# Performance work log

Measured on AMD Instinct MI355X. Metric: run time of the kernel, lower is better.

Reference implementation:

```python
import jax, jax.numpy as jnp
import numpy as np
from jax import lax

B, N, K, NCP = 4, 2048, 20, 400
EPS = 1e-5


def _bn(x, gamma, beta, axes):
    # training-mode batch norm (biased variance), channel axis = 1
    m = jnp.mean(x, axis=axes, keepdims=True)
    v = jnp.var(x, axis=axes, keepdims=True)
    shape = [1] * x.ndim
    shape[1] = -1
    return (x - m) * lax.rsqrt(v + EPS) * gamma.reshape(shape) + beta.reshape(shape)


def _knn_idx(x, k):
    # x: [B, C, N] -> idx [B, N, k] (nearest, includes self like torch.cdist+topk(largest=False))
    x2 = jnp.sum(x * x, axis=1)  # [B, N]
    d = x2[:, :, None] + x2[:, None, :] - 2.0 * jnp.einsum('bcn,bcm->bnm', x, x)
    return lax.top_k(-d, k)[1]


def _edge_conv(x, w, gamma, beta, k):
    # x: [B, C, N], w: [O, 2C] -> [B, O, N] (1x1 conv + BN + LeakyReLU + max over k)
    idx = _knn_idx(x, k)                      # [B, N, k]
    xt = jnp.transpose(x, (0, 2, 1))          # [B, N, C]
    b = jnp.arange(xt.shape[0])[:, None, None]
    nbr = xt[b, idx]                          # [B, N, k, C]
    ctr = xt[:, :, None, :]
    feat = jnp.concatenate([nbr - ctr, jnp.broadcast_to(ctr, nbr.shape)], axis=-1)  # [B, N, k, 2C]
    y = jnp.einsum('bnkc,oc->bonk', feat, w)  # [B, O, N, k]
    y = jax.nn.leaky_relu(_bn(y, gamma, beta, axes=(0, 2, 3)), 0.2)
    return jnp.max(y, axis=-1)                # [B, O, N]


def setup_inputs() -> dict:
    key = jax.random.key(0)
    ks = jax.random.split(key, 16)
    rnd = lambda k_, s: jax.random.normal(k_, s, dtype=jnp.float32) * 0.02
    inp = {
        'x': jax.random.normal(ks[0], (B, 3, N), dtype=jnp.float32),
        'w1': rnd(ks[1], (64, 6)),    'g1': jnp.ones(64),   'b1': jnp.zeros(64),
        'w2': rnd(ks[2], (128, 128)), 'g2': jnp.ones(128),  'b2': jnp.zeros(128),
        'w3': rnd(ks[3], (256, 256)), 'g3': jnp.ones(256),  'b3': jnp.zeros(256),
        'w4': rnd(ks[4], (512, 512)), 'g4': jnp.ones(512),  'b4': jnp.zeros(512),
        'w5': rnd(ks[5], (2048, 963)), 'g5': jnp.ones(2048), 'b5': jnp.zeros(2048),
        'w6': rnd(ks[6], (2048, 2048)), 'wb6': jnp.zeros(2048), 'g6': jnp.ones(2048), 'b6': jnp.zeros(2048),
        'w7': rnd(ks[7], (4096, 4096)), 'wb7': jnp.zeros(4096), 'g7': jnp.ones(4096), 'b7': jnp.zeros(4096),
        'w8': rnd(ks[8], (NCP, 4096)), 'wb8': jnp.zeros(NCP),
    }
    return inp


def reference(x, w1, g1, b1, w2, g2, b2, w3, g3, b3, w4, g4, b4,
              w5, g5, b5, w6, wb6, g6, b6, w7, wb7, g7, b7, w8, wb8):
    x0 = x                                            # [B, 3, N]
    x1 = _edge_conv(x0, w1, g1, b1, K)                # [B, 64, N]
    x2 = _edge_conv(x1, w2, g2, b2, K)                # [B, 128, N]
    x3 = _edge_conv(x2, w3, g3, b3, K)                # [B, 256, N]
    x4 = _edge_conv(x3, w4, g4, b4, K)                # [B, 512, N]
    h = jnp.concatenate([x0, x1, x2, x3, x4], axis=1) # [B, 963, N]
    h = jnp.einsum('bcn,oc->bon', h, w5)              # [B, 2048, N]
    h = jax.nn.leaky_relu(_bn(h, g5, b5, axes=(0, 2)), 0.2)
    p = jnp.max(h, axis=-1, keepdims=True)            # [B, 2048, 1] global max pool
    y = jnp.einsum('bcl,oc->bol', p, w6) + wb6[None, :, None]
    y = jax.nn.relu(_bn(y, g6, b6, axes=(0, 2)))
    y = jnp.concatenate([y, p], axis=1)               # [B, 4096, 1]
    y = jnp.einsum('bcl,oc->bol', y, w7) + wb7[None, :, None]
    y = jax.nn.relu(_bn(y, g7, b7, axes=(0, 2)))
    y = jnp.einsum('bcl,oc->bol', y, w8) + wb8[None, :, None]
    return jnp.tanh(y[:, :, 0])                       # [B, NCP]
```

## Files before the change

kernel.cpp:

```cpp
#include <hip/hip_runtime.h>
#include <float.h>
#include <math.h>


#define NPTS 2048
#define BATCH 4
#define KNN 20
#define CH_H 963
#define KPAD 992
#define HSTRIDE (CH_H*NPTS)

typedef _Float16 half8 __attribute__((ext_vector_type(8)));
typedef float f32x4 __attribute__((ext_vector_type(4)));

__device__ __forceinline__ unsigned fenc(float x){
  unsigned u = __float_as_uint(x);
  return (u & 0x80000000u) ? ~u : (u | 0x80000000u);
}
__device__ __forceinline__ float fdec(unsigned u){
  u = (u & 0x80000000u) ? (u ^ 0x80000000u) : ~u;
  return __uint_as_float(u);
}

__global__ void k_convert(const float* __restrict__ x, float* __restrict__ H){
  int i = blockIdx.x*256 + threadIdx.x;
  if (i >= BATCH*3*NPTS) return;
  int b = i / (3*NPTS); int r = i % (3*NPTS);
  H[(size_t)b*HSTRIDE + r] = x[i];
}

__global__ void k_norms(const float* __restrict__ X, int C, float* __restrict__ X2,
                        float* __restrict__ SUMZ){
  int i = blockIdx.x*256 + threadIdx.x;
  if (i < 1024) SUMZ[i] = 0.f;
  int b = i >> 11, n = i & 2047;
  const float* Xb = X + (size_t)b*HSTRIDE + n;
  float s = 0.f;
  for (int c=0;c<C;++c){ float v = Xb[(size_t)c*NPTS]; s = fmaf(v,v,s); }
  X2[i] = s;
}

__global__ __launch_bounds__(256) void k_xsplit(const float* __restrict__ X, int C, int Cpad,
        _Float16* __restrict__ Xhi, _Float16* __restrict__ Xlo)
{
  __shared__ float t[64][65];
  int b = blockIdx.z;
  int n0 = blockIdx.x*64, c0 = blockIdx.y*64;
  int tid = threadIdx.x; int l = tid & 63, m = tid >> 6;
  for (int cc = m; cc < 64; cc += 4){
    int c = c0 + cc;
    t[cc][l] = (c < C) ? X[(size_t)b*HSTRIDE + (size_t)c*NPTS + n0 + l] : 0.f;
  }
  __syncthreads();
  for (int nn = m; nn < 64; nn += 4){
    int c = c0 + l;
    if (c < Cpad){
      float v = t[l][nn];
      _Float16 h = (_Float16)v;
      size_t o = ((size_t)(b<<11)+n0+nn)*Cpad + c;
      Xhi[o] = h;
      Xlo[o] = (_Float16)(v - (float)h);
    }
  }
}

__global__ __launch_bounds__(256) void k_gram(const _Float16* __restrict__ Xhi,
        const _Float16* __restrict__ Xlo, int Cpad, int bbase,
        float* __restrict__ G0, float* __restrict__ G1)
{
  __shared__ half8 AsH[128][4]; __shared__ half8 AsL[128][4];
  __shared__ half8 BsH[128][4]; __shared__ half8 BsL[128][4];
  int bl = blockIdx.z;
  int b  = bbase + bl;
  float* G = bl ? G1 : G0;
  const _Float16* Hb = Xhi + (size_t)(b<<11)*Cpad;
  const _Float16* Lb = Xlo + (size_t)(b<<11)*Cpad;
  int m0 = blockIdx.x*128, n0 = blockIdx.y*128;
  int tid = threadIdx.x;
  int w = tid>>6, lane = tid&63;
  int wm = w>>1, wn = w&1;
  int quad = lane>>4, col = lane&15;
  f32x4 acc[4][4];
  #pragma unroll
  for (int i=0;i<4;++i)
    #pragma unroll
    for (int j=0;j<4;++j) acc[i][j] = (f32x4){0.f,0.f,0.f,0.f};

  for (int k0=0; k0<Cpad; k0+=32){
    #pragma unroll
    for (int h=0; h<2; ++h){
      int cid = tid + h*256;
      int row = cid>>2, kc = cid&3;
      size_t ao = (size_t)(n0+row)*Cpad + k0 + kc*8;
      size_t bo = (size_t)(m0+row)*Cpad + k0 + kc*8;
      AsH[row][kc] = *(const half8*)(Hb + ao);
      AsL[row][kc] = *(const half8*)(Lb + ao);
      BsH[row][kc] = *(const half8*)(Hb + bo);
      BsL[row][kc] = *(const half8*)(Lb + bo);
    }
    __syncthreads();
    half8 ah[4], al[4], bh[4], blo[4];
    #pragma unroll
    for (int mt=0;mt<4;++mt){ ah[mt] = AsH[wm*64 + mt*16 + col][quad];
                              al[mt] = AsL[wm*64 + mt*16 + col][quad]; }
    #pragma unroll
    for (int nt=0;nt<4;++nt){ bh[nt] = BsH[wn*64 + nt*16 + col][quad];
                              blo[nt] = BsL[wn*64 + nt*16 + col][quad]; }
    #pragma unroll
    for (int mt=0;mt<4;++mt)
      #pragma unroll
      for (int nt=0;nt<4;++nt){
        acc[mt][nt] = __builtin_amdgcn_mfma_f32_16x16x32_f16(ah[mt], bh[nt], acc[mt][nt], 0, 0, 0);
        acc[mt][nt] = __builtin_amdgcn_mfma_f32_16x16x32_f16(ah[mt], blo[nt], acc[mt][nt], 0, 0, 0);
        acc[mt][nt] = __builtin_amdgcn_mfma_f32_16x16x32_f16(al[mt], bh[nt], acc[mt][nt], 0, 0, 0);
      }
    __syncthreads();
  }
  #pragma unroll
  for (int mt=0;mt<4;++mt){
    #pragma unroll
    for (int r=0;r<4;++r){
      int n = n0 + wm*64 + mt*16 + quad*4 + r;
      #pragma unroll
      for (int nt=0;nt<4;++nt){
        int m = m0 + wn*64 + nt*16 + col;
        G[(size_t)n*2048 + m] = acc[mt][nt][r];
      }
    }
  }
}

#define KNN_CH(OPC) OPC(0) OPC(1) OPC(2) OPC(3) OPC(4) OPC(5) OPC(6) OPC(7)
#define DECL_CH(ch) float d##ch##_0,d##ch##_1,d##ch##_2,d##ch##_3;
#define LOADG_CH(ch) { float4 g = *(const float4*)(grow + (ch)*256 + base); \
  float4 xm = *(const float4*)(x2b + (ch)*256 + base); \
  d##ch##_0 = x2n + xm.x - 2.f*g.x; d##ch##_1 = x2n + xm.y - 2.f*g.y; \
  d##ch##_2 = x2n + xm.z - 2.f*g.z; d##ch##_3 = x2n + xm.w - 2.f*g.w; }
#define DECL_G(ch) float gv##ch; int gm##ch;
#define MKCH(ch) { gv##ch = d##ch##_0; gm##ch = (ch)*256 + base; \
  if (d##ch##_1 < gv##ch){ gv##ch = d##ch##_1; gm##ch = (ch)*256 + base + 1; } \
  if (d##ch##_2 < gv##ch){ gv##ch = d##ch##_2; gm##ch = (ch)*256 + base + 2; } \
  if (d##ch##_3 < gv##ch){ gv##ch = d##ch##_3; gm##ch = (ch)*256 + base + 3; } }
#define REMCASE(ch) case ch: { \
  if (own){ if (cp==0) d##ch##_0 = FLT_MAX; else if (cp==1) d##ch##_1 = FLT_MAX; \
            else if (cp==2) d##ch##_2 = FLT_MAX; else d##ch##_3 = FLT_MAX; } \
  MKCH(ch) } break;

__global__ __launch_bounds__(256,4) void k_sel(const float* __restrict__ G0,
        const float* __restrict__ G1, const float* __restrict__ X2,
        int bbase, int* __restrict__ IDX)
{
  int tid = threadIdx.x;
  int w = tid >> 6, lane = tid & 63;
  int n = blockIdx.x*4 + w;
  int b = bbase + blockIdx.y;
  const float* grow = (blockIdx.y ? G1 : G0) + (size_t)n*2048;
  const float* x2b  = X2 + (b<<11);
  float x2n = x2b[n];
  int base = lane << 2;
  KNN_CH(DECL_CH)
  KNN_CH(LOADG_CH)
  KNN_CH(DECL_G)
  KNN_CH(MKCH)
  int* op = IDX + ((size_t)(b<<11)+n)*KNN;
  for (int it=0; it<KNN; ++it){
    float v = fminf(fminf(fminf(gv0,gv1),fminf(gv2,gv3)),
                    fminf(fminf(gv4,gv5),fminf(gv6,gv7)));
    #pragma unroll
    for (int s=1; s<64; s<<=1) v = fminf(v, __shfl_xor(v, s));
    int mc = 0x7fffffff;
    mc = (gv7==v) ? gm7 : mc;
    mc = (gv6==v) ? gm6 : mc;
    mc = (gv5==v) ? gm5 : mc;
    mc = (gv4==v) ? gm4 : mc;
    mc = (gv3==v) ? gm3 : mc;
    mc = (gv2==v) ? gm2 : mc;
    mc = (gv1==v) ? gm1 : mc;
    mc = (gv0==v) ? gm0 : mc;
    int m = mc;
    #pragma unroll
    for (int s=1; s<64; s<<=1) m = min(m, __shfl_xor(m, s));
    if (lane==0) op[it] = m;
    int sm = __builtin_amdgcn_readfirstlane(m);
    bool own = (lane == ((sm>>2)&63));
    int cp = sm & 3;
    switch (sm >> 8){ KNN_CH(REMCASE) }
  }
}

__global__ __launch_bounds__(256) void k_vu(const float* __restrict__ X,
        const float* __restrict__ W, int C, int O,
        float* __restrict__ V, float* __restrict__ U)
{
  __shared__ float Xs[8][128];
  __shared__ float Wdv[8][64];
  __shared__ float Wuv[8][64];
  int b = blockIdx.z, n0 = blockIdx.x*128, o0 = blockIdx.y*64;
  int tid = threadIdx.x;
  int tj = tid & 15, ti = tid >> 4;
  float4 aV[8], aU[8];
  #pragma unroll
  for (int i=0;i<8;++i){ aV[i]=make_float4(0,0,0,0); aU[i]=make_float4(0,0,0,0); }
  const float* Xb = X + (size_t)b*HSTRIDE;
  for (int c0=0;c0<C;c0+=8){
    {
      int cc = tid >> 5, nn = (tid & 31) * 4; int c = c0 + cc;
      float4 v = (c<C) ? *(const float4*)(Xb + (size_t)c*NPTS + n0 + nn)
                       : make_float4(0,0,0,0);
      *(float4*)&Xs[cc][nn] = v;
    }
    for (int l=tid;l<512;l+=256){
      int oo=l>>3, cc=l&7, c=c0+cc;
      float wd=0.f, wu=0.f;
      if (c<C){
        const float* wr = W + (size_t)(o0+oo)*(2*C);
        wd = wr[c]; wu = wr[C+c] - wd;
      }
      Wdv[cc][oo]=wd; Wuv[cc][oo]=wu;
    }
    __syncthreads();
    #pragma unroll
    for (int cc=0;cc<8;++cc){
      float4 x0 = *(float4*)&Xs[cc][ti*8];
      float4 x1 = *(float4*)&Xs[cc][ti*8+4];
      float4 wd = *(float4*)&Wdv[cc][tj*4];
      float4 wu = *(float4*)&Wuv[cc][tj*4];
      float xs[8] = {x0.x,x0.y,x0.z,x0.w,x1.x,x1.y,x1.z,x1.w};
      #pragma unroll
      for (int i=0;i<8;++i){
        aV[i].x = fmaf(xs[i], wd.x, aV[i].x);
        aV[i].y = fmaf(xs[i], wd.y, aV[i].y);
        aV[i].z = fmaf(xs[i], wd.z, aV[i].z);
        aV[i].w = fmaf(xs[i], wd.w, aV[i].w);
        aU[i].x = fmaf(xs[i], wu.x, aU[i].x);
        aU[i].y = fmaf(xs[i], wu.y, aU[i].y);
        aU[i].z = fmaf(xs[i], wu.z, aU[i].z);
        aU[i].w = fmaf(xs[i], wu.w, aU[i].w);
      }
    }
    __syncthreads();
  }
  #pragma unroll
  for (int i=0;i<8;++i){
    int n = n0 + ti*8 + i;
    size_t basep = ((size_t)b*NPTS + n)*O + o0 + tj*4;
    *(float4*)(V+basep) = aV[i];
    *(float4*)(U+basep) = aU[i];
  }
}

__global__ __launch_bounds__(256) void k_gather(const float* __restrict__ V, const float* __restrict__ U,
        const int* __restrict__ IDX, int O,
        float* __restrict__ YMX, float* __restrict__ YMN,
        float* __restrict__ SUM, float* __restrict__ SUMSQ)
{
  const int NT = 8;
  __shared__ int sidx[NT*KNN];
  int bi = blockIdx.x;
  int b  = bi >> 8;
  int n0 = (bi & 255) * NT;
  int tid = threadIdx.x;
  for (int l = tid; l < NT*KNN; l += 256)
    sidx[l] = IDX[((size_t)(b<<11)+n0)*KNN + l];
  __syncthreads();
  int othr  = (O < 256) ? O : 256;
  int o0    = tid & (othr-1);
  int ns    = tid / othr;
  int nstep = 256 / othr;
  for (int o = o0; o < O; o += othr){
    float s = 0.f, q = 0.f;
    for (int nn = ns; nn < NT; nn += nstep){
      int n = n0 + nn;
      size_t ub = ((size_t)(b<<11)+n)*O + o;
      float u = U[ub];
      float mx = -FLT_MAX, mn = FLT_MAX;
      #pragma unroll
      for (int k=0;k<KNN;++k){
        int m = sidx[nn*KNN+k];
        float y = V[((size_t)(b<<11)+m)*O + o] + u;
        mx = fmaxf(mx,y); mn = fminf(mn,y);
        s += y; q = fmaf(y,y,q);
      }
      YMX[ub] = mx; YMN[ub] = mn;
    }
    atomicAdd(&SUM[o], s); atomicAdd(&SUMSQ[o], q);
  }
}

__global__ void k_finalize(const float* __restrict__ SUM, const float* __restrict__ SUMSQ,
        const float* __restrict__ g, const float* __restrict__ bt,
        int O, float invM, float* __restrict__ SC, float* __restrict__ SH){
  int o = blockIdx.x*256 + threadIdx.x;
  if (o>=O) return;
  float m = SUM[o]*invM;
  float var = SUMSQ[o]*invM - m*m;
  float sc = g[o] * rsqrtf(var + 1e-5f);
  SC[o]=sc; SH[o] = bt[o] - m*sc;
}

__global__ __launch_bounds__(256) void k_apply(const float* __restrict__ YMX, const float* __restrict__ YMN,
        const float* __restrict__ SC, const float* __restrict__ SH,
        int O, float* __restrict__ OUT)
{
  __shared__ float t[64][65];
  int b = blockIdx.z;
  int o0 = blockIdx.y*64, n0 = blockIdx.x*64;
  int tid = threadIdx.x;
  int lo = tid & 63, ln = tid >> 6;
  float sc = SC[o0+lo], sh = SH[o0+lo];
  for (int nn = ln; nn < 64; nn += 4){
    size_t idx = ((size_t)(b<<11)+n0+nn)*O + o0 + lo;
    float v = (sc >= 0.f) ? YMX[idx] : YMN[idx];
    float y = fmaf(sc, v, sh);
    y = (y > 0.f) ? y : 0.2f*y;
    t[lo][nn] = y;
  }
  __syncthreads();
  for (int oo = ln; oo < 64; oo += 4){
    OUT[(size_t)b*HSTRIDE + (size_t)(o0+oo)*NPTS + n0 + lo] = t[oo][lo];
  }
}

__global__ __launch_bounds__(256) void k_h2f16(const float* __restrict__ H, _Float16* __restrict__ Hf){
  __shared__ float t[64][65];
  int b = blockIdx.z;
  int n0 = blockIdx.x*64, c0 = blockIdx.y*64;
  int tid = threadIdx.x; int l = tid & 63, m = tid >> 6;
  for (int cc = m; cc < 64; cc += 4){
    int c = c0 + cc;
    t[cc][l] = (c < CH_H) ? H[(size_t)b*HSTRIDE + (size_t)c*NPTS + n0 + l] : 0.f;
  }
  __syncthreads();
  for (int nn = m; nn < 64; nn += 4){
    int c = c0 + l;
    if (c < KPAD)
      Hf[((size_t)(b<<11)+n0+nn)*KPAD + c] = (_Float16)t[l][nn];
  }
}

__global__ void k_w5f16(const float* __restrict__ w5, _Float16* __restrict__ Wf,
                        unsigned* __restrict__ z){
  int i = blockIdx.x*256 + threadIdx.x;
  if (i < 12288) z[i] = 0u;
  else if (i < 20480) z[i] = 0xFFFFFFFFu;
  if (i >= 2048*KPAD) return;
  int o = i / KPAD, c = i - o*KPAD;
  Wf[i] = (c < CH_H) ? (_Float16)w5[(size_t)o*CH_H + c] : (_Float16)0.f;
}

__global__ __launch_bounds__(256) void k_l5mfma(const _Float16* __restrict__ Wf,
        const _Float16* __restrict__ Hf,
        float* __restrict__ SUM5, float* __restrict__ SUMSQ5,
        unsigned* __restrict__ MAXB, unsigned* __restrict__ MINB)
{
  __shared__ half8 As[128][4];
  __shared__ half8 Bs[128][4];
  int b  = blockIdx.z;
  int n0 = blockIdx.x*128, o0 = blockIdx.y*128;
  int tid = threadIdx.x;
  int w = tid>>6, lane = tid&63;
  int wm = w>>1, wn = w&1;
  int quad = lane>>4, col = lane&15;
  f32x4 acc[4][4];
  #pragma unroll
  for (int i=0;i<4;++i)
    #pragma unroll
    for (int j=0;j<4;++j) acc[i][j] = (f32x4){0.f,0.f,0.f,0.f};

  for (int k0=0; k0<KPAD; k0+=32){
    #pragma unroll
    for (int h=0; h<2; ++h){
      int cid = tid + h*256;
      int row = cid>>2, kc = cid&3;
      As[row][kc] = *(const half8*)(Wf + (size_t)(o0+row)*KPAD + k0 + kc*8);
      Bs[row][kc] = *(const half8*)(Hf + ((size_t)(b<<11)+n0+row)*KPAD + k0 + kc*8);
    }
    __syncthreads();
    half8 af[4], bf[4];
    #pragma unroll
    for (int mt=0;mt<4;++mt) af[mt] = As[wm*64 + mt*16 + col][quad];
    #pragma unroll
    for (int nt=0;nt<4;++nt) bf[nt] = Bs[wn*64 + nt*16 + col][quad];
    #pragma unroll
    for (int mt=0;mt<4;++mt)
      #pragma unroll
      for (int nt=0;nt<4;++nt)
        acc[mt][nt] = __builtin_amdgcn_mfma_f32_16x16x32_f16(af[mt], bf[nt], acc[mt][nt], 0, 0, 0);
    __syncthreads();
  }
  #pragma unroll
  for (int mt=0;mt<4;++mt){
    #pragma unroll
    for (int r=0;r<4;++r){
      float s=0.f, q=0.f, mx=-FLT_MAX, mn=FLT_MAX;
      #pragma unroll
      for (int nt=0;nt<4;++nt){
        float y = acc[mt][nt][r];
        s += y; q = fmaf(y,y,q);
        mx = fmaxf(mx,y); mn = fminf(mn,y);
      }
      #pragma unroll
      for (int d=8; d; d>>=1){
        s += __shfl_down(s,(unsigned)d,16);
        q += __shfl_down(q,(unsigned)d,16);
        mx = fmaxf(mx,__shfl_down(mx,(unsigned)d,16));
        mn = fminf(mn,__shfl_down(mn,(unsigned)d,16));
      }
      if (col==0){
        int o = o0 + wm*64 + mt*16 + quad*4 + r;
        atomicAdd(&SUM5[o], s);
        atomicAdd(&SUMSQ5[o], q);
        atomicMax(&MAXB[(b<<11)+o], fenc(mx));
        atomicMin(&MINB[(b<<11)+o], fenc(mn));
      }
    }
  }
}

__global__ void k_l5_final(const float* __restrict__ SUM5, const float* __restrict__ SUMSQ5,
        const unsigned* __restrict__ MAXB, const unsigned* __restrict__ MINB,
        const float* __restrict__ g5, const float* __restrict__ b5, float* __restrict__ P)
{
  int o = blockIdx.x*256 + threadIdx.x;
  if (o>=2048) return;
  float m = SUM5[o]*(1.f/8192.f);
  float var = SUMSQ5[o]*(1.f/8192.f) - m*m;
  float sc = g5[o] * rsqrtf(var + 1e-5f);
  float sh = b5[o] - m*sc;
  for (int b=0;b<4;++b){
    float mx = fdec(MAXB[b*2048+o]);
    float mn = fdec(MINB[b*2048+o]);
    float v = (sc >= 0.f) ? fmaf(sc,mx,sh) : fmaf(sc,mn,sh);
    v = (v > 0.f) ? v : 0.2f*v;
    P[b*2048 + o] = v;
  }
}

__global__ __launch_bounds__(256) void k_fc(const float* __restrict__ W, const float* __restrict__ bias,
        const float* __restrict__ Z, int Cin, int O, float* __restrict__ Y)
{
  int o = blockIdx.x*4 + (threadIdx.x>>6);
  int lane = threadIdx.x & 63;
  if (o >= O) return;
  const float* wr = W + (size_t)o*Cin;
  float a0=0.f,a1=0.f,a2=0.f,a3=0.f;
  for (int c=lane;c<Cin;c+=64){
    float w = wr[c];
    a0 = fmaf(w, Z[c],        a0);
    a1 = fmaf(w, Z[Cin+c],    a1);
    a2 = fmaf(w, Z[2*Cin+c],  a2);
    a3 = fmaf(w, Z[3*Cin+c],  a3);
  }
  #pragma unroll
  for (int s=32;s;s>>=1){
    a0 += __shfl_down(a0,(unsigned)s); a1 += __shfl_down(a1,(unsigned)s);
    a2 += __shfl_down(a2,(unsigned)s); a3 += __shfl_down(a3,(unsigned)s);
  }
  if (lane==0){
    float bb = bias[o];
    Y[o]=a0+bb; Y[O+o]=a1+bb; Y[2*O+o]=a2+bb; Y[3*O+o]=a3+bb;
  }
}

__global__ void k_bn4(const float* __restrict__ Y, const float* __restrict__ g, const float* __restrict__ bt,
                      int O, float* __restrict__ Z, int zstride, int zoff)
{
  int o = blockIdx.x*256 + threadIdx.x;
  if (o>=O) return;
  float v0=Y[o], v1=Y[O+o], v2=Y[2*O+o], v3=Y[3*O+o];
  float m = 0.25f*(v0+v1+v2+v3);
  float d0=v0-m, d1=v1-m, d2=v2-m, d3=v3-m;
  float var = 0.25f*(d0*d0+d1*d1+d2*d2+d3*d3);
  float sc = g[o] * rsqrtf(var + 1e-5f);
  float sh = bt[o] - m*sc;
  Z[0*zstride+zoff+o] = fmaxf(fmaf(sc,v0,sh), 0.f);
  Z[1*zstride+zoff+o] = fmaxf(fmaf(sc,v1,sh), 0.f);
  Z[2*zstride+zoff+o] = fmaxf(fmaf(sc,v2,sh), 0.f);
  Z[3*zstride+zoff+o] = fmaxf(fmaf(sc,v3,sh), 0.f);
}

__global__ void k_copy_p(const float* __restrict__ P, float* __restrict__ Z){
  int i = blockIdx.x*256 + threadIdx.x;
  int b = i>>11, o = i&2047;
  Z[b*4096 + 2048 + o] = P[i];
}

__global__ __launch_bounds__(256) void k_final(const float* __restrict__ W8, const float* __restrict__ wb8,
        const float* __restrict__ Z7, float* __restrict__ out)
{
  int o = blockIdx.x*4 + (threadIdx.x>>6);
  int lane = threadIdx.x & 63;
  if (o >= 400) return;
  const float* wr = W8 + (size_t)o*4096;
  float a0=0.f,a1=0.f,a2=0.f,a3=0.f;
  for (int c=lane;c<4096;c+=64){
    float w = wr[c];
    a0 = fmaf(w, Z7[c],        a0);
    a1 = fmaf(w, Z7[4096+c],   a1);
    a2 = fmaf(w, Z7[2*4096+c], a2);
    a3 = fmaf(w, Z7[3*4096+c], a3);
  }
  #pragma unroll
  for (int s=32;s;s>>=1){
    a0 += __shfl_down(a0,(unsigned)s); a1 += __shfl_down(a1,(unsigned)s);
    a2 += __shfl_down(a2,(unsigned)s); a3 += __shfl_down(a3,(unsigned)s);
  }
  if (lane==0){
    float bb = wb8[o];
    out[0*400+o] = tanhf(a0+bb);
    out[1*400+o] = tanhf(a1+bb);
    out[2*400+o] = tanhf(a2+bb);
    out[3*400+o] = tanhf(a3+bb);
  }
}

extern "C" void kernel_launch(void* const* d_in, const int* in_sizes, int n_in,
                              void* d_out, int out_size, void* d_ws, size_t ws_size,
                              hipStream_t stream)
{
  const float* x   = (const float*)d_in[0];
  const float* w_e[4]  = {(const float*)d_in[1], (const float*)d_in[4], (const float*)d_in[7], (const float*)d_in[10]};
  const float* g_e[4]  = {(const float*)d_in[2], (const float*)d_in[5], (const float*)d_in[8], (const float*)d_in[11]};
  const float* b_e[4]  = {(const float*)d_in[3], (const float*)d_in[6], (const float*)d_in[9], (const float*)d_in[12]};
  const float* w5  = (const float*)d_in[13];
  const float* g5  = (const float*)d_in[14];
  const float* b5  = (const float*)d_in[15];
  const float* w6  = (const float*)d_in[16];
  const float* wb6 = (const float*)d_in[17];
  const float* g6  = (const float*)d_in[18];
  const float* b6  = (const float*)d_in[19];
  const float* w7  = (const float*)d_in[20];
  const float* wb7 = (const float*)d_in[21];
  const float* g7  = (const float*)d_in[22];
  const float* b7  = (const float*)d_in[23];
  const float* w8  = (const float*)d_in[24];
  const float* wb8 = (const float*)d_in[25];

  float* WS = (float*)d_ws;
  float* H    = WS;
  float* V    = WS + 7888896;
  float* U    = V  + 4194304;
  float* YMX  = U  + 4194304;
  float* YMN  = YMX+ 4194304;
  int*   IDX  = (int*)(YMN + 4194304);
  float* X2   = (float*)(IDX + 163840);
  float* SUM  = X2 + 8192;
  float* SUMSQ= SUM + 512;
  float* SC   = SUMSQ + 512;
  float* SH   = SC + 512;
  float* SUM5 = SH + 512;
  float* SUMSQ5 = SUM5 + 2048;
  unsigned* MAXB = (unsigned*)(SUMSQ5 + 2048);
  unsigned* MINB = MAXB + 8192;
  float* P    = (float*)(MINB + 8192);
  float* Y6   = P + 8192;
  float* Z    = Y6 + 8192;
  float* Y7   = Z + 16384;
  float* Z7   = Y7 + 16384;
  _Float16* Hf  = (_Float16*)V;
  _Float16* Wf  = (_Float16*)U;
  _Float16* Xhi = (_Float16*)U;
  _Float16* Xlo = (_Float16*)U + 4*2048*256;
  float* G0 = YMX;
  float* G1 = YMN;

  k_convert<<<96,256,0,stream>>>(x, H);

  const int Cin_[4]  = {3,64,128,256};
  const int Cpad_[4] = {32,64,128,256};
  const int O_[4]    = {64,128,256,512};
  const int ioff_[4] = {0,3,67,195};
  const int ooff_[4] = {3,67,195,451};

  for (int l=0;l<4;++l){
    const float* Xl = H + (size_t)ioff_[l]*NPTS;
    int C = Cin_[l], Cpad = Cpad_[l], O = O_[l];
    k_norms<<<32,256,0,stream>>>(Xl, C, X2, SUM);
    dim3 gxs(32, (Cpad+63)/64, 4);
    k_xsplit<<<gxs,256,0,stream>>>(Xl, C, Cpad, Xhi, Xlo);
    dim3 ggr(16,16,2);
    k_gram<<<ggr,256,0,stream>>>(Xhi, Xlo, Cpad, 0, G0, G1);
    dim3 gsl(512,2);
    k_sel<<<gsl,256,0,stream>>>(G0, G1, X2, 0, IDX);
    k_gram<<<ggr,256,0,stream>>>(Xhi, Xlo, Cpad, 2, G0, G1);
    k_sel<<<gsl,256,0,stream>>>(G0, G1, X2, 2, IDX);
    dim3 gvu(16, O/64, 4);
    k_vu<<<gvu,256,0,stream>>>(Xl, w_e[l], C, O, V, U);
    k_gather<<<1024,256,0,stream>>>(V, U, IDX, O, YMX, YMN, SUM, SUMSQ);
    k_finalize<<<2,256,0,stream>>>(SUM, SUMSQ, g_e[l], b_e[l], O, 1.f/163840.f, SC, SH);
    dim3 gap(32, O/64, 4);
    k_apply<<<gap,256,0,stream>>>(YMX, YMN, SC, SH, O, H + (size_t)ooff_[l]*NPTS);
  }

  dim3 gtr(32,16,4);
  k_h2f16<<<gtr,256,0,stream>>>(H, Hf);
  k_w5f16<<<(2048*KPAD+255)/256,256,0,stream>>>(w5, Wf, (unsigned*)SUM5);
  dim3 g5g(16,16,4);
  k_l5mfma<<<g5g,256,0,stream>>>(Wf, Hf, SUM5, SUMSQ5, MAXB, MINB);
  k_l5_final<<<8,256,0,stream>>>(SUM5, SUMSQ5, MAXB, MINB, g5, b5, P);

  k_fc<<<512,256,0,stream>>>(w6, wb6, P, 2048, 2048, Y6);
  k_bn4<<<8,256,0,stream>>>(Y6, g6, b6, 2048, Z, 4096, 0);
  k_copy_p<<<32,256,0,stream>>>(P, Z);
  k_fc<<<1024,256,0,stream>>>(w7, wb7, Z, 4096, 4096, Y7);
  k_bn4<<<16,256,0,stream>>>(Y7, g7, b7, 4096, Z7, 4096, 0);
  k_final<<<100,256,0,stream>>>(w8, wb8, Z7, (float*)d_out);
}
```

Measured before the change: 1.193 ms.

## Exploit Gram symmetry, fuse distance computation into gram, fold BN finalize into apply

The gram kernel now launches only lower-triangular 128x128 tiles (136 per batch) and writes each tile plus its transpose. It also computes the full squared distance x2n+x2m-2g in its epilogue, so the selection kernel just loads distances. The separate BN finalize kernel is removed and its scale/shift computation is done inside k_apply. This roughly halves the gram MFMA work and drops one launch per layer, at the cost of strided, uncoalesced transposed stores in the gram epilogue.

```diff
diff --git a/kernel.cpp b/kernel.cpp
--- a/kernel.cpp
+++ b/kernel.cpp
@@ -65,17 +65,22 @@
 }
 
 __global__ __launch_bounds__(256) void k_gram(const _Float16* __restrict__ Xhi,
-        const _Float16* __restrict__ Xlo, int Cpad, int bbase,
-        float* __restrict__ G0, float* __restrict__ G1)
+        const _Float16* __restrict__ Xlo, const float* __restrict__ X2,
+        int Cpad, int bbase, float* __restrict__ D0, float* __restrict__ D1)
 {
   __shared__ half8 AsH[128][4]; __shared__ half8 AsL[128][4];
   __shared__ half8 BsH[128][4]; __shared__ half8 BsL[128][4];
   int bl = blockIdx.z;
   int b  = bbase + bl;
-  float* G = bl ? G1 : G0;
+  float* D = bl ? D1 : D0;
+  int t = blockIdx.x;
+  int r = (int)((sqrtf((float)(8*t+1)) - 1.f) * 0.5f);
+  while ((r+1)*(r+2)/2 <= t) ++r;
+  while (r*(r+1)/2 > t) --r;
+  int c = t - r*(r+1)/2;
+  int n0 = r*128, m0 = c*128;
   const _Float16* Hb = Xhi + (size_t)(b<<11)*Cpad;
   const _Float16* Lb = Xlo + (size_t)(b<<11)*Cpad;
-  int m0 = blockIdx.x*128, n0 = blockIdx.y*128;
   int tid = threadIdx.x;
   int w = tid>>6, lane = tid&63;
   int wm = w>>1, wn = w&1;
@@ -116,15 +121,19 @@
       }
     __syncthreads();
   }
+  const float* x2b = X2 + (b<<11);
   #pragma unroll
   for (int mt=0;mt<4;++mt){
     #pragma unroll
-    for (int r=0;r<4;++r){
-      int n = n0 + wm*64 + mt*16 + quad*4 + r;
+    for (int r2=0;r2<4;++r2){
+      int n = n0 + wm*64 + mt*16 + quad*4 + r2;
+      float x2n = x2b[n];
       #pragma unroll
       for (int nt=0;nt<4;++nt){
         int m = m0 + wn*64 + nt*16 + col;
-        G[(size_t)n*2048 + m] = acc[mt][nt][r];
+        float d = x2n + x2b[m] - 2.f*acc[mt][nt][r2];
+        D[(size_t)n*2048 + m] = d;
+        D[(size_t)m*2048 + n] = d;
       }
     }
   }
@@ -132,10 +141,8 @@
 
 #define KNN_CH(OPC) OPC(0) OPC(1) OPC(2) OPC(3) OPC(4) OPC(5) OPC(6) OPC(7)
 #define DECL_CH(ch) float d##ch##_0,d##ch##_1,d##ch##_2,d##ch##_3;
-#define LOADG_CH(ch) { float4 g = *(const float4*)(grow + (ch)*256 + base); \
-  float4 xm = *(const float4*)(x2b + (ch)*256 + base); \
-  d##ch##_0 = x2n + xm.x - 2.f*g.x; d##ch##_1 = x2n + xm.y - 2.f*g.y; \
-  d##ch##_2 = x2n + xm.z - 2.f*g.z; d##ch##_3 = x2n + xm.w - 2.f*g.w; }
+#define LOADD_CH(ch) { float4 g4 = *(const float4*)(drow + (ch)*256 + base); \
+  d##ch##_0 = g4.x; d##ch##_1 = g4.y; d##ch##_2 = g4.z; d##ch##_3 = g4.w; }
 #define DECL_G(ch) float gv##ch; int gm##ch;
 #define MKCH(ch) { gv##ch = d##ch##_0; gm##ch = (ch)*256 + base; \
   if (d##ch##_1 < gv##ch){ gv##ch = d##ch##_1; gm##ch = (ch)*256 + base + 1; } \
@@ -146,20 +153,17 @@
             else if (cp==2) d##ch##_2 = FLT_MAX; else d##ch##_3 = FLT_MAX; } \
   MKCH(ch) } break;
 
-__global__ __launch_bounds__(256,4) void k_sel(const float* __restrict__ G0,
-        const float* __restrict__ G1, const float* __restrict__ X2,
-        int bbase, int* __restrict__ IDX)
+__global__ __launch_bounds__(256,4) void k_sel(const float* __restrict__ D0,
+        const float* __restrict__ D1, int bbase, int* __restrict__ IDX)
 {
   int tid = threadIdx.x;
   int w = tid >> 6, lane = tid & 63;
   int n = blockIdx.x*4 + w;
   int b = bbase + blockIdx.y;
-  const float* grow = (blockIdx.y ? G1 : G0) + (size_t)n*2048;
-  const float* x2b  = X2 + (b<<11);
-  float x2n = x2b[n];
+  const float* drow = (blockIdx.y ? D1 : D0) + (size_t)n*2048;
   int base = lane << 2;
   KNN_CH(DECL_CH)
-  KNN_CH(LOADG_CH)
+  KNN_CH(LOADD_CH)
   KNN_CH(DECL_G)
   KNN_CH(MKCH)
   int* op = IDX + ((size_t)(b<<11)+n)*KNN;
@@ -287,29 +291,23 @@
   }
 }
 
-__global__ void k_finalize(const float* __restrict__ SUM, const float* __restrict__ SUMSQ,
+__global__ __launch_bounds__(256) void k_apply(const float* __restrict__ YMX, const float* __restrict__ YMN,
+        const float* __restrict__ SUM, const float* __restrict__ SUMSQ,
         const float* __restrict__ g, const float* __restrict__ bt,
-        int O, float invM, float* __restrict__ SC, float* __restrict__ SH){
-  int o = blockIdx.x*256 + threadIdx.x;
-  if (o>=O) return;
-  float m = SUM[o]*invM;
-  float var = SUMSQ[o]*invM - m*m;
-  float sc = g[o] * rsqrtf(var + 1e-5f);
-  SC[o]=sc; SH[o] = bt[o] - m*sc;
-}
-
-__global__ __launch_bounds__(256) void k_apply(const float* __restrict__ YMX, const float* __restrict__ YMN,
-        const float* __restrict__ SC, const float* __restrict__ SH,
-        int O, float* __restrict__ OUT)
+        int O, float invM, float* __restrict__ OUT)
 {
   __shared__ float t[64][65];
   int b = blockIdx.z;
   int o0 = blockIdx.y*64, n0 = blockIdx.x*64;
   int tid = threadIdx.x;
   int lo = tid & 63, ln = tid >> 6;
-  float sc = SC[o0+lo], sh = SH[o0+lo];
+  int o = o0 + lo;
+  float m = SUM[o]*invM;
+  float var = SUMSQ[o]*invM - m*m;
+  float sc = g[o] * rsqrtf(var + 1e-5f);
+  float sh = bt[o] - m*sc;
   for (int nn = ln; nn < 64; nn += 4){
-    size_t idx = ((size_t)(b<<11)+n0+nn)*O + o0 + lo;
+    size_t idx = ((size_t)(b<<11)+n0+nn)*O + o;
     float v = (sc >= 0.f) ? YMX[idx] : YMN[idx];
     float y = fmaf(sc, v, sh);
     y = (y > 0.f) ? y : 0.2f*y;
@@ -546,9 +544,7 @@
   float* X2   = (float*)(IDX + 163840);
   float* SUM  = X2 + 8192;
   float* SUMSQ= SUM + 512;
-  float* SC   = SUMSQ + 512;
-  float* SH   = SC + 512;
-  float* SUM5 = SH + 512;
+  float* SUM5 = SUMSQ + 512;
   float* SUMSQ5 = SUM5 + 2048;
   unsigned* MAXB = (unsigned*)(SUMSQ5 + 2048);
   unsigned* MINB = MAXB + 8192;
@@ -561,8 +557,8 @@
   _Float16* Wf  = (_Float16*)U;
   _Float16* Xhi = (_Float16*)U;
   _Float16* Xlo = (_Float16*)U + 4*2048*256;
-  float* G0 = YMX;
-  float* G1 = YMN;
+  float* D0 = YMX;
+  float* D1 = YMN;
 
   k_convert<<<96,256,0,stream>>>(x, H);
 
@@ -578,18 +574,18 @@
     k_norms<<<32,256,0,stream>>>(Xl, C, X2, SUM);
     dim3 gxs(32, (Cpad+63)/64, 4);
     k_xsplit<<<gxs,256,0,stream>>>(Xl, C, Cpad, Xhi, Xlo);
-    dim3 ggr(16,16,2);
-    k_gram<<<ggr,256,0,stream>>>(Xhi, Xlo, Cpad, 0, G0, G1);
+    dim3 ggr(136, 1, 2);
+    k_gram<<<ggr,256,0,stream>>>(Xhi, Xlo, X2, Cpad, 0, D0, D1);
     dim3 gsl(512,2);
-    k_sel<<<gsl,256,0,stream>>>(G0, G1, X2, 0, IDX);
-    k_gram<<<ggr,256,0,stream>>>(Xhi, Xlo, Cpad, 2, G0, G1);
-    k_sel<<<gsl,256,0,stream>>>(G0, G1, X2, 2, IDX);
+    k_sel<<<gsl,256,0,stream>>>(D0, D1, 0, IDX);
+    k_gram<<<ggr,256,0,stream>>>(Xhi, Xlo, X2, Cpad, 2, D0, D1);
+    k_sel<<<gsl,256,0,stream>>>(D0, D1, 2, IDX);
     dim3 gvu(16, O/64, 4);
     k_vu<<<gvu,256,0,stream>>>(Xl, w_e[l], C, O, V, U);
     k_gather<<<1024,256,0,stream>>>(V, U, IDX, O, YMX, YMN, SUM, SUMSQ);
-    k_finalize<<<2,256,0,stream>>>(SUM, SUMSQ, g_e[l], b_e[l], O, 1.f/163840.f, SC, SH);
     dim3 gap(32, O/64, 4);
-    k_apply<<<gap,256,0,stream>>>(YMX, YMN, SC, SH, O, H + (size_t)ooff_[l]*NPTS);
+    k_apply<<<gap,256,0,stream>>>(YMX, YMN, SUM, SUMSQ, g_e[l], b_e[l], O,
+                                  1.f/163840.f, H + (size_t)ooff_[l]*NPTS);
   }
 
   dim3 gtr(32,16,4);
```

Result: slower. 1.294 ms (+8.5%).
